# Kernel optimization log

Hardware: AMD Instinct MI355X
Metric: run time of the kernel (lower is better)

Reference implementation:

```python
import jax, jax.numpy as jnp
import numpy as np

IN_F = 4096
OUT_F = 4096
C = 32            # num_codebooks
NCL = 32          # n_clusters
SUB = IN_F // C   # 128, per-codebook sub-dim
CLS = OUT_F // NCL  # 128, cluster_size
SIGMA = 10.0
THRESH = 0.5


def setup_inputs() -> dict:
    key = jax.random.key(0)
    ks = jax.random.split(key, 6)
    x = jax.random.normal(ks[0], (4, 2048, IN_F), dtype=jnp.float32)
    # RPQ codebooks: (C, 256, SUB), init normal(0, 0.025)
    codebooks = jax.random.normal(ks[1], (C, 256, SUB), dtype=jnp.float32) * 0.025
    # centroids: (n_clusters, C) uint8 codes, stored transposed as (C, n_clusters)
    centroids = jax.random.randint(ks[2], (NCL, C), 0, 256, dtype=jnp.int32)
    codes = jnp.repeat(centroids, CLS, axis=0)  # (OUT_F, C)
    n_pert = max(1, round(0.25 * C))
    psel = jax.random.randint(ks[3], (OUT_F, n_pert), 0, C, dtype=jnp.int32)
    prep = jax.random.randint(ks[4], (OUT_F, n_pert), 0, 256, dtype=jnp.int32)
    rows = jnp.arange(OUT_F)[:, None]
    codes = codes.at[rows, psel].set(prep)
    bound = 1.0 / np.sqrt(IN_F)
    bias = jax.random.uniform(ks[5], (OUT_F,), dtype=jnp.float32, minval=-bound, maxval=bound)
    ln_weight = jnp.ones((NCL,), dtype=jnp.float32) * SIGMA
    return {
        "x": x,
        "codebooks": codebooks,
        "bias": bias,
        "ln_weight": ln_weight,
        "codes": codes.T.astype(jnp.int32),        # (C, OUT_F)
        "centroids": centroids.T.astype(jnp.int32),  # (C, NCL)
    }


def _expand(codes, codebooks):
    # codes: (C, N) int; codebooks: (C, 256, SUB) -> weight (N, C*SUB)
    w = codebooks[jnp.arange(codes.shape[0])[:, None], codes]  # (C, N, SUB)
    return jnp.transpose(w, (1, 0, 2)).reshape(codes.shape[1], -1)


def reference(x, codebooks, bias, ln_weight, codes, centroids):
    shape = x.shape
    x2 = x.reshape(-1, shape[-1])  # (n, IN_F)
    # key_search: input-centroid dots, layer norm (no bias), softmax
    cw = _expand(centroids, codebooks)            # (NCL, IN_F)
    dots = x2 @ cw.T                              # (n, NCL)
    mu = jnp.mean(dots, axis=-1, keepdims=True)
    var = jnp.var(dots, axis=-1, keepdims=True)
    dots = (dots - mu) * jax.lax.rsqrt(var + 1e-5) * ln_weight
    soft = jax.nn.softmax(dots, axis=-1)
    m = soft > THRESH                             # (n, NCL)
    qmask = jnp.any(m, axis=-1)                   # selected queries
    cmask = jnp.any(m, axis=0)                    # selected clusters
    kmask = jnp.repeat(cmask, CLS)                # (OUT_F,) indices=arange reshaped
    # sparse linear + scatter == dense linear masked to (selected q) x (selected k)
    W = _expand(codes, codebooks)                 # (OUT_F, IN_F)
    y = x2 @ W.T + bias                           # (n, OUT_F)
    y = y * (qmask[:, None] & kmask[None, :]).astype(y.dtype)
    return y.reshape(*shape[:-1], OUT_F)
```

## Files before the change

### kernel.cpp

```cpp
#include <hip/hip_runtime.h>
#include <hip/hip_bf16.h>
#include <stdint.h>

#define IN_F 4096
#define OUT_F 4096
#define NCLUST 32
#define MROWS 8192

typedef __attribute__((ext_vector_type(8))) short bf16x8;
typedef __attribute__((ext_vector_type(4))) float f32x4;

#define OFF_CMASK ((size_t)0)
#define OFF_QTILE ((size_t)256)
#define OFF_QMASK ((size_t)1024)
#define OFF_WHI   ((size_t)65536)
#define OFF_WLO   ((size_t)(65536 + 262144))
#define OFF_XB    ((size_t)1 << 20)
#define OFF_WB    (((size_t)1 << 20) + (size_t)MROWS * IN_F * 2)

__device__ __forceinline__ void gload_lds16(const void* g, void* l) {
  __builtin_amdgcn_global_load_lds(
      (const __attribute__((address_space(1))) void*)g,
      (__attribute__((address_space(3))) void*)l, 16, 0, 0);
}

__global__ void k0b_fragw(const float* __restrict__ codebooks,
                          const int* __restrict__ centroids,
                          uint4* __restrict__ whi, uint4* __restrict__ wlo,
                          int* __restrict__ cmask, int* __restrict__ qtile) {
  int gid = blockIdx.x * 256 + threadIdx.x;
  int l = gid & 63;
  int ct = (gid >> 6) & 1;
  int ks = gid >> 7;
  int c = ct * 16 + (l & 15);
  int k0 = ks * 32 + 8 * (l >> 4);
  int sub = k0 >> 7;
  int off = k0 & 127;
  int idx = centroids[sub * 32 + c];
  const float* src = codebooks + ((size_t)(sub * 256 + idx)) * 128 + off;
  float4 v0 = *(const float4*)src;
  float4 v1 = *(const float4*)(src + 4);
  float f[8] = {v0.x, v0.y, v0.z, v0.w, v1.x, v1.y, v1.z, v1.w};
  union { __hip_bfloat16 b[8]; uint4 q; } uh, ul;
  #pragma unroll
  for (int i = 0; i < 8; ++i) {
    __hip_bfloat16 h = __float2bfloat16(f[i]);
    uh.b[i] = h;
    ul.b[i] = __float2bfloat16(f[i] - __bfloat162float(h));
  }
  whi[gid] = uh.q;
  wlo[gid] = ul.q;
  if (gid < 32) cmask[gid] = 0;
  else if (gid < 96) qtile[gid - 32] = 0;
}

__global__ __launch_bounds__(256) void k1_dots(
    const float* __restrict__ x,
    const uint4* __restrict__ whi4, const uint4* __restrict__ wlo4,
    const float* __restrict__ lnw,
    __hip_bfloat16* __restrict__ xb,
    int* __restrict__ qmask, int* __restrict__ cmask, int* __restrict__ qtile) {
  __shared__ __align__(16) float xsf[32 * 256];
  __shared__ float part[4][32][32];
  const int t = threadIdx.x;
  const int wv = t >> 6;
  const int l = t & 63;
  const size_t row0 = (size_t)blockIdx.x * 32;
  const float* xg = x + row0 * IN_F;
  const bf16x8* whif = (const bf16x8*)whi4;
  const bf16x8* wlof = (const bf16x8*)wlo4;

  f32x4 zz = {0.f, 0.f, 0.f, 0.f};
  f32x4 acc[2][2];
  acc[0][0] = zz; acc[0][1] = zz; acc[1][0] = zz; acc[1][1] = zz;

  const int col = (t & 63) * 4;
  float4 reg[8];
  #pragma unroll
  for (int j = 0; j < 8; ++j)
    reg[j] = *(const float4*)&xg[(size_t)(4 * j + wv) * IN_F + col];

  for (int ch = 0; ch < 16; ++ch) {
    #pragma unroll
    for (int j = 0; j < 8; ++j) {
      int row = 4 * j + wv;
      int sw = (row & 7) << 2;
      *(float4*)&xsf[row * 256 + (col ^ sw)] = reg[j];
      union { __hip_bfloat16 b[4]; uint2 q; } u;
      u.b[0] = __float2bfloat16(reg[j].x);
      u.b[1] = __float2bfloat16(reg[j].y);
      u.b[2] = __float2bfloat16(reg[j].z);
      u.b[3] = __float2bfloat16(reg[j].w);
      *(uint2*)&xb[(row0 + row) * IN_F + ch * 256 + col] = u.q;
    }
    if (ch + 1 < 16) {
      #pragma unroll
      for (int j = 0; j < 8; ++j)
        reg[j] = *(const float4*)&xg[(size_t)(4 * j + wv) * IN_F + (ch + 1) * 256 + col];
    }
    __syncthreads();
    #pragma unroll
    for (int s = 0; s < 2; ++s) {
      int kk = wv * 64 + s * 32 + 8 * (l >> 4);
      int gk = ch * 8 + wv * 2 + s;
      bf16x8 ahi[2], alo[2];
      #pragma unroll
      for (int rt = 0; rt < 2; ++rt) {
        int row = rt * 16 + (l & 15);
        int sw = (row & 7) << 2;
        float4 f0 = *(const float4*)&xsf[row * 256 + (kk ^ sw)];
        float4 f1 = *(const float4*)&xsf[row * 256 + ((kk ^ sw) ^ 4)];
        float f[8] = {f0.x, f0.y, f0.z, f0.w, f1.x, f1.y, f1.z, f1.w};
        union { __hip_bfloat16 b[8]; bf16x8 v; } uh, ul;
        #pragma unroll
        for (int i = 0; i < 8; ++i) {
          __hip_bfloat16 h = __float2bfloat16(f[i]);
          uh.b[i] = h;
          ul.b[i] = __float2bfloat16(f[i] - __bfloat162float(h));
        }
        ahi[rt] = uh.v; alo[rt] = ul.v;
      }
      #pragma unroll
      for (int ct = 0; ct < 2; ++ct) {
        bf16x8 bh = whif[(gk * 2 + ct) * 64 + l];
        bf16x8 bl = wlof[(gk * 2 + ct) * 64 + l];
        #pragma unroll
        for (int rt = 0; rt < 2; ++rt) {
          acc[rt][ct] = __builtin_amdgcn_mfma_f32_16x16x32_bf16(ahi[rt], bh, acc[rt][ct], 0, 0, 0);
          acc[rt][ct] = __builtin_amdgcn_mfma_f32_16x16x32_bf16(ahi[rt], bl, acc[rt][ct], 0, 0, 0);
          acc[rt][ct] = __builtin_amdgcn_mfma_f32_16x16x32_bf16(alo[rt], bh, acc[rt][ct], 0, 0, 0);
        }
      }
    }
    __syncthreads();
  }

  #pragma unroll
  for (int rt = 0; rt < 2; ++rt)
    #pragma unroll
    for (int ct = 0; ct < 2; ++ct)
      #pragma unroll
      for (int j = 0; j < 4; ++j) {
        int row = rt * 16 + (l >> 4) * 4 + j;
        int cc = ct * 16 + (l & 15);
        part[wv][row][cc] = acc[rt][ct][j];
      }
  __syncthreads();

  #pragma unroll
  for (int rg = 0; rg < 4; ++rg) {
    int r = rg * 8 + (t >> 5);
    int c = t & 31;
    float d = part[0][r][c] + part[1][r][c] + part[2][r][c] + part[3][r][c];
    float s1 = d;
    for (int m = 1; m < 32; m <<= 1) s1 += __shfl_xor(s1, m);
    float mu = s1 * (1.f / 32.f);
    float dv = d - mu;
    float s2 = dv * dv;
    for (int m = 1; m < 32; m <<= 1) s2 += __shfl_xor(s2, m);
    float var = s2 * (1.f / 32.f);
    float nd = dv * (1.f / sqrtf(var + 1e-5f)) * lnw[c];
    float mx = nd;
    for (int m = 1; m < 32; m <<= 1) mx = fmaxf(mx, __shfl_xor(mx, m));
    float e = expf(nd - mx);
    float se = e;
    for (int m = 1; m < 32; m <<= 1) se += __shfl_xor(se, m);
    bool hit = (e / se) > 0.5f;
    if (hit) atomicOr(&cmask[c], 1);
    int h = hit ? 1 : 0;
    for (int m = 1; m < 32; m <<= 1) h |= __shfl_xor(h, m);
    if (c == 0) {
      size_t row = row0 + r;
      qmask[row] = h;
      if (h) atomicOr(&qtile[row >> 7], 1);
    }
  }
}

__global__ void k2_expand_w(const float* __restrict__ codebooks,
                            const int* __restrict__ codes,
                            __hip_bfloat16* __restrict__ wb) {
  const int o = blockIdx.x;
  const int tid = threadIdx.x;
  #pragma unroll
  for (int it = 0; it < 2; ++it) {
    int i0 = (it * 256 + tid) * 8;
    int c = i0 >> 7;
    int s = i0 & 127;
    int idx = codes[c * OUT_F + o];
    const float* src = codebooks + ((size_t)(c * 256 + idx)) * 128 + s;
    float4 v0 = *(const float4*)src;
    float4 v1 = *(const float4*)(src + 4);
    union { __hip_bfloat16 b[8]; uint4 q; } u;
    u.b[0] = __float2bfloat16(v0.x); u.b[1] = __float2bfloat16(v0.y);
    u.b[2] = __float2bfloat16(v0.z); u.b[3] = __float2bfloat16(v0.w);
    u.b[4] = __float2bfloat16(v1.x); u.b[5] = __float2bfloat16(v1.y);
    u.b[6] = __float2bfloat16(v1.z); u.b[7] = __float2bfloat16(v1.w);
    *(uint4*)&wb[(size_t)o * IN_F + i0] = u.q;
  }
}


__global__ __launch_bounds__(512, 2) void k3_gemm(
    const __hip_bfloat16* __restrict__ A,
    const __hip_bfloat16* __restrict__ B,
    const float* __restrict__ bias,
    const int* __restrict__ qmask, const int* __restrict__ cmask,
    const int* __restrict__ qtile,
    float* __restrict__ out) {
  __shared__ char smem[131072];
  const int tid = threadIdx.x;
  const int bid = blockIdx.x;
  const int swz = (bid & 7) * 64 + (bid >> 3);
  const int bm = swz >> 4;
  const int bn = swz & 15;
  const int m0 = bm * 256;
  const int n0 = bn * 256;

  const int cmA = cmask[bn * 2], cmB = cmask[bn * 2 + 1];
  if ((qtile[bm * 2] | qtile[bm * 2 + 1]) == 0 || (cmA | cmB) == 0) {
    float4 z = make_float4(0.f, 0.f, 0.f, 0.f);
    for (int i = tid; i < 256 * 64; i += 512) {
      int rr = i >> 6;
      int cc = (i & 63) << 2;
      *(float4*)&out[((size_t)(m0 + rr)) * OUT_F + n0 + cc] = z;
    }
    return;
  }

  const int w = tid >> 6;
  const int l = tid & 63;
  const int wm = w >> 2;
  const int wn = w & 3;
  const int wmo = wm * 64;
  const int wno = wn * 32;
  const int lr = l & 15;
  const int g = l >> 4;
  const int lb = l & 7;
  const int r8 = l >> 3;
  const int csw = ((l & 7) ^ r8) << 4;
  const size_t rowb = (size_t)IN_F * 2;

  const char* Asrc = (const char*)A + (size_t)(m0 + w * 8 + r8) * rowb + csw;
  const char* Bsrc = (const char*)B + (size_t)(n0 + w * 8 + r8) * rowb + csw;

#define STAGE_A(b, h, j, t) gload_lds16( \
    Asrc + (size_t)((h)*128 + (j)*64) * rowb + (size_t)(t) * 128, \
    smem + (b)*32768 + ((h)*128 + (j)*64 + w*8) * 128)
#define STAGE_B(b, h, j, t) gload_lds16( \
    Bsrc + (size_t)((h)*128 + (j)*64) * rowb + (size_t)(t) * 128, \
    smem + 65536 + (b)*32768 + ((h)*128 + (j)*64 + w*8) * 128)

#define VM4 asm volatile("s_waitcnt vmcnt(4)" ::: "memory")
#define VMN

#define PHASE(MH, NH, BUF, STAGES, VMW) do { \
    bf16x8 af[4][2], bfq[2][2]; \
    const char* sAb = smem + (BUF) * 32768; \
    const char* sBb = smem + 65536 + (BUF) * 32768; \
    _Pragma("unroll") \
    for (int mi = 0; mi < 4; ++mi) { \
      int R = (MH)*128 + wmo + mi*16 + lr; \
      int c0 = ((g ^ lb) << 4); \
      af[mi][0] = *(const bf16x8*)(sAb + R*128 + c0); \
      af[mi][1] = *(const bf16x8*)(sAb + R*128 + (((4 + g) ^ lb) << 4)); \
    } \
    _Pragma("unroll") \
    for (int ni = 0; ni < 2; ++ni) { \
      int R = (NH)*128 + wno + ni*16 + lr; \
      bfq[ni][0] = *(const bf16x8*)(sBb + R*128 + ((g ^ lb) << 4)); \
      bfq[ni][1] = *(const bf16x8*)(sBb + R*128 + (((4 + g) ^ lb) << 4)); \
    } \
    STAGES; \
    VMW; \
    __builtin_amdgcn_sched_barrier(0); \
    __builtin_amdgcn_s_barrier(); \
    asm volatile("s_waitcnt lgkmcnt(0)" ::: "memory"); \
    __builtin_amdgcn_sched_barrier(0); \
    __builtin_amdgcn_s_setprio(1); \
    _Pragma("unroll") \
    for (int mi = 0; mi < 4; ++mi) \
      _Pragma("unroll") \
      for (int ni = 0; ni < 2; ++ni) { \
        acc[MH][NH][mi][ni] = __builtin_amdgcn_mfma_f32_16x16x32_bf16( \
            af[mi][0], bfq[ni][0], acc[MH][NH][mi][ni], 0, 0, 0); \
        acc[MH][NH][mi][ni] = __builtin_amdgcn_mfma_f32_16x16x32_bf16( \
            af[mi][1], bfq[ni][1], acc[MH][NH][mi][ni], 0, 0, 0); \
      } \
    __builtin_amdgcn_s_setprio(0); \
    __builtin_amdgcn_s_barrier(); \
  } while (0)

  f32x4 zz = {0.f, 0.f, 0.f, 0.f};
  f32x4 acc[2][2][4][2];
  #pragma unroll
  for (int a = 0; a < 2; ++a)
    #pragma unroll
    for (int b = 0; b < 2; ++b)
      #pragma unroll
      for (int c = 0; c < 4; ++c)
        #pragma unroll
        for (int d = 0; d < 2; ++d) acc[a][b][c][d] = zz;

  STAGE_A(0, 0, 0, 0); STAGE_A(0, 0, 1, 0);
  STAGE_B(0, 0, 0, 0); STAGE_B(0, 0, 1, 0);
  STAGE_A(0, 1, 0, 0); STAGE_A(0, 1, 1, 0);
  STAGE_B(0, 1, 0, 0); STAGE_B(0, 1, 1, 0);
  STAGE_A(1, 0, 0, 1); STAGE_A(1, 0, 1, 1);
  STAGE_B(1, 0, 0, 1); STAGE_B(1, 0, 1, 1);
  asm volatile("s_waitcnt vmcnt(4)" ::: "memory");
  __builtin_amdgcn_s_barrier();

  for (int i = 0; i < 32; ++i) {
    const int t1 = 2 * i + 1;
    const int t2 = (2 * i + 2) & 63;
    const int t3 = (2 * i + 3) & 63;
    PHASE(0, 0, 0, { STAGE_A(1,1,0,t1); STAGE_A(1,1,1,t1); STAGE_B(1,1,0,t1); STAGE_B(1,1,1,t1); }, VMN);
    PHASE(0, 1, 0, {}, VMN);
    PHASE(1, 0, 0, { STAGE_A(0,0,0,t2); STAGE_A(0,0,1,t2); }, VMN);
    PHASE(1, 1, 0, { STAGE_B(0,0,0,t2); STAGE_B(0,0,1,t2); }, VM4);
    PHASE(0, 0, 1, { STAGE_A(0,1,0,t2); STAGE_A(0,1,1,t2); STAGE_B(0,1,0,t2); STAGE_B(0,1,1,t2); }, VMN);
    PHASE(0, 1, 1, {}, VMN);
    PHASE(1, 0, 1, { STAGE_A(1,0,0,t3); STAGE_A(1,0,1,t3); }, VMN);
    PHASE(1, 1, 1, { STAGE_B(1,0,0,t3); STAGE_B(1,0,1,t3); }, VM4);
  }

  asm volatile("s_waitcnt vmcnt(0)" ::: "memory");

  const int g4 = g * 4;
  #pragma unroll
  for (int MH = 0; MH < 2; ++MH) {
    #pragma unroll
    for (int mi = 0; mi < 4; ++mi) {
      #pragma unroll
      for (int j = 0; j < 4; ++j) {
        int row = m0 + MH * 128 + wmo + mi * 16 + g4 + j;
        float qm = qmask[row] ? 1.f : 0.f;
        float fA = qm * (cmA ? 1.f : 0.f);
        float fB = qm * (cmB ? 1.f : 0.f);
        #pragma unroll
        for (int NH = 0; NH < 2; ++NH) {
          float fc = NH ? fB : fA;
          #pragma unroll
          for (int ni = 0; ni < 2; ++ni) {
            int col = n0 + NH * 128 + wno + ni * 16 + lr;
            out[(size_t)row * OUT_F + col] =
                (acc[MH][NH][mi][ni][j] + bias[col]) * fc;
          }
        }
      }
    }
  }
#undef PHASE
#undef STAGE_A
#undef STAGE_B
#undef VM4
#undef VMN
}

extern "C" void kernel_launch(void* const* d_in, const int* in_sizes, int n_in,
                              void* d_out, int out_size, void* d_ws, size_t ws_size,
                              hipStream_t stream) {
  const float* x = (const float*)d_in[0];
  const float* codebooks = (const float*)d_in[1];
  const float* bias = (const float*)d_in[2];
  const float* lnw = (const float*)d_in[3];
  const int* codes = (const int*)d_in[4];
  const int* centroids = (const int*)d_in[5];
  float* out = (float*)d_out;

  char* ws = (char*)d_ws;
  int* cmask = (int*)(ws + OFF_CMASK);
  int* qtile = (int*)(ws + OFF_QTILE);
  int* qmask = (int*)(ws + OFF_QMASK);
  uint4* whi = (uint4*)(ws + OFF_WHI);
  uint4* wlo = (uint4*)(ws + OFF_WLO);
  __hip_bfloat16* xb = (__hip_bfloat16*)(ws + OFF_XB);
  __hip_bfloat16* wb = (__hip_bfloat16*)(ws + OFF_WB);

  hipLaunchKernelGGL(k0b_fragw, dim3(64), dim3(256), 0, stream,
                     codebooks, centroids, whi, wlo, cmask, qtile);
  hipLaunchKernelGGL(k1_dots, dim3(256), dim3(256), 0, stream,
                     x, whi, wlo, lnw, xb, qmask, cmask, qtile);
  hipLaunchKernelGGL(k2_expand_w, dim3(4096), dim3(256), 0, stream,
                     codebooks, codes, wb);
  hipLaunchKernelGGL(k3_gemm, dim3(512), dim3(512), 0, stream,
                     xb, wb, bias, qmask, cmask, qtile, out);
}
```

Measured before the change: 532.7 us.

## Split x conversion out of dots kernel and read x directly in dots

Moves the fp32->bf16 conversion of x into a separate grid-stride kernel. The dots kernel now uses 8 waves that load x fragments straight from global memory instead of staging through LDS with block syncs. The aim is to remove the LDS staging and synchronisation overhead and to raise parallelism in the key-search kernel. In exchange, x is read from memory twice.

Result: no change. 531.2 us (-0.3%).

```diff
diff --git a/kernel.cpp b/kernel.cpp
--- a/kernel.cpp
+++ b/kernel.cpp
@@ -54,19 +54,33 @@
   else if (gid < 96) qtile[gid - 32] = 0;
 }
 
-__global__ __launch_bounds__(256) void k1_dots(
+__global__ __launch_bounds__(256) void k1a_convert(const float* __restrict__ x,
+                                                   __hip_bfloat16* __restrict__ xb) {
+  size_t i = ((size_t)blockIdx.x * 256 + threadIdx.x) * 8;
+  const size_t stride = (size_t)gridDim.x * 256 * 8;
+  const size_t total = (size_t)MROWS * IN_F;
+  for (; i < total; i += stride) {
+    float4 v0 = *(const float4*)&x[i];
+    float4 v1 = *(const float4*)&x[i + 4];
+    union { __hip_bfloat16 b[8]; uint4 q; } u;
+    u.b[0] = __float2bfloat16(v0.x); u.b[1] = __float2bfloat16(v0.y);
+    u.b[2] = __float2bfloat16(v0.z); u.b[3] = __float2bfloat16(v0.w);
+    u.b[4] = __float2bfloat16(v1.x); u.b[5] = __float2bfloat16(v1.y);
+    u.b[6] = __float2bfloat16(v1.z); u.b[7] = __float2bfloat16(v1.w);
+    *(uint4*)&xb[i] = u.q;
+  }
+}
+
+__global__ __launch_bounds__(512) void k1b_dots(
     const float* __restrict__ x,
     const uint4* __restrict__ whi4, const uint4* __restrict__ wlo4,
     const float* __restrict__ lnw,
-    __hip_bfloat16* __restrict__ xb,
     int* __restrict__ qmask, int* __restrict__ cmask, int* __restrict__ qtile) {
-  __shared__ __align__(16) float xsf[32 * 256];
-  __shared__ float part[4][32][32];
+  __shared__ float part[8][32][32];
   const int t = threadIdx.x;
   const int wv = t >> 6;
   const int l = t & 63;
   const size_t row0 = (size_t)blockIdx.x * 32;
-  const float* xg = x + row0 * IN_F;
   const bf16x8* whif = (const bf16x8*)whi4;
   const bf16x8* wlof = (const bf16x8*)wlo4;
 
@@ -74,65 +88,39 @@
   f32x4 acc[2][2];
   acc[0][0] = zz; acc[0][1] = zz; acc[1][0] = zz; acc[1][1] = zz;
 
-  const int col = (t & 63) * 4;
-  float4 reg[8];
-  #pragma unroll
-  for (int j = 0; j < 8; ++j)
-    reg[j] = *(const float4*)&xg[(size_t)(4 * j + wv) * IN_F + col];
-
-  for (int ch = 0; ch < 16; ++ch) {
-    #pragma unroll
-    for (int j = 0; j < 8; ++j) {
-      int row = 4 * j + wv;
-      int sw = (row & 7) << 2;
-      *(float4*)&xsf[row * 256 + (col ^ sw)] = reg[j];
-      union { __hip_bfloat16 b[4]; uint2 q; } u;
-      u.b[0] = __float2bfloat16(reg[j].x);
-      u.b[1] = __float2bfloat16(reg[j].y);
-      u.b[2] = __float2bfloat16(reg[j].z);
-      u.b[3] = __float2bfloat16(reg[j].w);
-      *(uint2*)&xb[(row0 + row) * IN_F + ch * 256 + col] = u.q;
-    }
-    if (ch + 1 < 16) {
-      #pragma unroll
-      for (int j = 0; j < 8; ++j)
-        reg[j] = *(const float4*)&xg[(size_t)(4 * j + wv) * IN_F + (ch + 1) * 256 + col];
-    }
-    __syncthreads();
-    #pragma unroll
-    for (int s = 0; s < 2; ++s) {
-      int kk = wv * 64 + s * 32 + 8 * (l >> 4);
-      int gk = ch * 8 + wv * 2 + s;
-      bf16x8 ahi[2], alo[2];
+  const int lrow = l & 15;
+  const int kgrp = (l >> 4) * 8;
+
+  for (int ks = 0; ks < 16; ++ks) {
+    const int gk = wv * 16 + ks;
+    const int kb = gk * 32 + kgrp;
+    bf16x8 ahi[2], alo[2];
+    #pragma unroll
+    for (int rt = 0; rt < 2; ++rt) {
+      const float* src = &x[(row0 + rt * 16 + lrow) * IN_F + kb];
+      float4 f0 = *(const float4*)src;
+      float4 f1 = *(const float4*)(src + 4);
+      float f[8] = {f0.x, f0.y, f0.z, f0.w, f1.x, f1.y, f1.z, f1.w};
+      union { __hip_bfloat16 b[8]; bf16x8 v; } uh, ul;
+      #pragma unroll
+      for (int i = 0; i < 8; ++i) {
+        __hip_bfloat16 h = __float2bfloat16(f[i]);
+        uh.b[i] = h;
+        ul.b[i] = __float2bfloat16(f[i] - __bfloat162float(h));
+      }
+      ahi[rt] = uh.v; alo[rt] = ul.v;
+    }
+    #pragma unroll
+    for (int ct = 0; ct < 2; ++ct) {
+      bf16x8 bh = whif[(gk * 2 + ct) * 64 + l];
+      bf16x8 bl = wlof[(gk * 2 + ct) * 64 + l];
       #pragma unroll
       for (int rt = 0; rt < 2; ++rt) {
-        int row = rt * 16 + (l & 15);
-        int sw = (row & 7) << 2;
-        float4 f0 = *(const float4*)&xsf[row * 256 + (kk ^ sw)];
-        float4 f1 = *(const float4*)&xsf[row * 256 + ((kk ^ sw) ^ 4)];
-        float f[8] = {f0.x, f0.y, f0.z, f0.w, f1.x, f1.y, f1.z, f1.w};
-        union { __hip_bfloat16 b[8]; bf16x8 v; } uh, ul;
-        #pragma unroll
-        for (int i = 0; i < 8; ++i) {
-          __hip_bfloat16 h = __float2bfloat16(f[i]);
-          uh.b[i] = h;
-          ul.b[i] = __float2bfloat16(f[i] - __bfloat162float(h));
-        }
-        ahi[rt] = uh.v; alo[rt] = ul.v;
+        acc[rt][ct] = __builtin_amdgcn_mfma_f32_16x16x32_bf16(ahi[rt], bh, acc[rt][ct], 0, 0, 0);
+        acc[rt][ct] = __builtin_amdgcn_mfma_f32_16x16x32_bf16(ahi[rt], bl, acc[rt][ct], 0, 0, 0);
+        acc[rt][ct] = __builtin_amdgcn_mfma_f32_16x16x32_bf16(alo[rt], bh, acc[rt][ct], 0, 0, 0);
       }
-      #pragma unroll
-      for (int ct = 0; ct < 2; ++ct) {
-        bf16x8 bh = whif[(gk * 2 + ct) * 64 + l];
-        bf16x8 bl = wlof[(gk * 2 + ct) * 64 + l];
-        #pragma unroll
-        for (int rt = 0; rt < 2; ++rt) {
-          acc[rt][ct] = __builtin_amdgcn_mfma_f32_16x16x32_bf16(ahi[rt], bh, acc[rt][ct], 0, 0, 0);
-          acc[rt][ct] = __builtin_amdgcn_mfma_f32_16x16x32_bf16(ahi[rt], bl, acc[rt][ct], 0, 0, 0);
-          acc[rt][ct] = __builtin_amdgcn_mfma_f32_16x16x32_bf16(alo[rt], bh, acc[rt][ct], 0, 0, 0);
-        }
-      }
-    }
-    __syncthreads();
+    }
   }
 
   #pragma unroll
@@ -148,10 +136,12 @@
   __syncthreads();
 
   #pragma unroll
-  for (int rg = 0; rg < 4; ++rg) {
-    int r = rg * 8 + (t >> 5);
+  for (int pass = 0; pass < 2; ++pass) {
+    int r = pass * 16 + (t >> 5);
     int c = t & 31;
-    float d = part[0][r][c] + part[1][r][c] + part[2][r][c] + part[3][r][c];
+    float d = 0.f;
+    #pragma unroll
+    for (int w8 = 0; w8 < 8; ++w8) d += part[w8][r][c];
     float s1 = d;
     for (int m = 1; m < 32; m <<= 1) s1 += __shfl_xor(s1, m);
     float mu = s1 * (1.f / 32.f);
@@ -199,7 +189,6 @@
     *(uint4*)&wb[(size_t)o * IN_F + i0] = u.q;
   }
 }
-
 
 __global__ __launch_bounds__(512, 2) void k3_gemm(
     const __hip_bfloat16* __restrict__ A,
@@ -380,8 +369,10 @@
 
   hipLaunchKernelGGL(k0b_fragw, dim3(64), dim3(256), 0, stream,
                      codebooks, centroids, whi, wlo, cmask, qtile);
-  hipLaunchKernelGGL(k1_dots, dim3(256), dim3(256), 0, stream,
-                     x, whi, wlo, lnw, xb, qmask, cmask, qtile);
+  hipLaunchKernelGGL(k1b_dots, dim3(256), dim3(512), 0, stream,
+                     x, whi, wlo, lnw, qmask, cmask, qtile);
+  hipLaunchKernelGGL(k1a_convert, dim3(2048), dim3(256), 0, stream,
+                     x, xb);
   hipLaunchKernelGGL(k2_expand_w, dim3(4096), dim3(256), 0, stream,
                      codebooks, codes, wb);
   hipLaunchKernelGGL(k3_gemm, dim3(512), dim3(512), 0, stream,
```
